# Performance work log

Hardware: AMD Instinct MI355X
Metric: run time of the kernel (lower is better)

Reference implementation:

```python
import jax, jax.numpy as jnp
import numpy as np

B, T, F, H = 256, 128, 512, 512

def setup_inputs() -> dict:
    key = jax.random.key(0)
    ks = jax.random.split(key, 6)
    s_in = 1.0 / np.sqrt(F)
    s_rec = 1.0 / np.sqrt(H)
    return {
        "x": jax.random.normal(ks[0], (B, T, F), dtype=jnp.float32),
        "kernel": jax.random.uniform(ks[1], (F, 3 * H), jnp.float32, -s_in, s_in),
        "rec_kernel": jax.random.uniform(ks[2], (H, 3 * H), jnp.float32, -s_rec, s_rec),
        "bias": jnp.zeros((2, 3 * H), dtype=jnp.float32),  # [input_bias, recurrent_bias] (reset_after=True)
        "Wd": jax.random.uniform(ks[3], (H, 1), jnp.float32, -s_rec, s_rec),
        "bd": jnp.zeros((1,), dtype=jnp.float32),
    }

def reference(x, kernel, rec_kernel, bias, Wd, bd):
    # Keras GRU, reset_after=True, activation=relu, recurrent_activation=sigmoid.
    bi, br = bias[0], bias[1]
    # Precompute all input projections: [T, B, 3H]
    xp = jnp.swapaxes(jnp.einsum('btf,fg->btg', x, kernel) + bi, 0, 1)
    h0 = jnp.zeros((x.shape[0], rec_kernel.shape[0]), dtype=x.dtype)

    def step(h, xp_t):
        rec = h @ rec_kernel + br                  # [B, 3H]
        xz, xr, xh = jnp.split(xp_t, 3, axis=-1)
        rz, rr, rh = jnp.split(rec, 3, axis=-1)
        z = jax.nn.sigmoid(xz + rz)                # update gate
        r = jax.nn.sigmoid(xr + rr)                # reset gate
        hh = jax.nn.relu(xh + r * rh)              # candidate (relu activation)
        h_new = z * h + (1.0 - z) * hh
        return h_new, None

    hT, _ = jax.lax.scan(step, h0, xp)
    # Dropout(0.2) is identity at inference. Dense head:
    return hT @ Wd + bd
```

## Files before the change

kernel.cpp:

```cpp
#include <hip/hip_runtime.h>
#include <hip/hip_bf16.h>
#include <math.h>

constexpr int BATCH = 256;
constexpr int SEQ   = 128;
constexpr int FEAT  = 512;
constexpr int HID   = 512;
constexpr int G3    = 1536;

typedef __bf16 bf16x8 __attribute__((ext_vector_type(8)));
typedef float  f32x4  __attribute__((ext_vector_type(4)));
typedef int    i32x4v __attribute__((ext_vector_type(4)));

__global__ __launch_bounds__(256) void convert_bf16(
    const float* __restrict__ in, __hip_bfloat16* __restrict__ out, int n)
{
  int i = (blockIdx.x * 256 + threadIdx.x) * 8;
  if (i >= n) return;
  float4 v0 = *(const float4*)&in[i];
  float4 v1 = *(const float4*)&in[i + 4];
  __hip_bfloat16 o[8];
  o[0] = (__hip_bfloat16)v0.x; o[1] = (__hip_bfloat16)v0.y;
  o[2] = (__hip_bfloat16)v0.z; o[3] = (__hip_bfloat16)v0.w;
  o[4] = (__hip_bfloat16)v1.x; o[5] = (__hip_bfloat16)v1.y;
  o[6] = (__hip_bfloat16)v1.z; o[7] = (__hip_bfloat16)v1.w;
  *(int4*)&out[i] = *(int4*)o;
}

__global__ __launch_bounds__(256) void transpose_convert(
    const float* __restrict__ in, __hip_bfloat16* __restrict__ outT)
{
  __shared__ float tile[32][33];
  const int c0 = blockIdx.x * 32;
  const int r0 = blockIdx.y * 32;
  const int tid = threadIdx.x;
  {
    int row = tid >> 3, c4 = tid & 7;
    float4 v = *(const float4*)&in[(size_t)(r0 + row) * G3 + c0 + c4 * 4];
    tile[row][c4 * 4 + 0] = v.x;
    tile[row][c4 * 4 + 1] = v.y;
    tile[row][c4 * 4 + 2] = v.z;
    tile[row][c4 * 4 + 3] = v.w;
  }
  __syncthreads();
  {
    int rowT = tid >> 3, c4 = tid & 7;
    __hip_bfloat16 o[4];
#pragma unroll
    for (int e = 0; e < 4; ++e)
      o[e] = (__hip_bfloat16)tile[c4 * 4 + e][rowT];
    *(int2*)&outT[(size_t)(c0 + rowT) * FEAT + r0 + c4 * 4] = *(int2*)o;
  }
}

__global__ __launch_bounds__(256, 3) void proj_mfma(
    const __hip_bfloat16* __restrict__ xb, const __hip_bfloat16* __restrict__ WkT,
    const float* __restrict__ bias, __hip_bfloat16* __restrict__ xp)
{
  __shared__ __align__(16) __hip_bfloat16 As[128 * 64];
  __shared__ __align__(16) __hip_bfloat16 Bs[128 * 64];

  const int tid = threadIdx.x;
  const int wave = tid >> 6, l = tid & 63;
  const int wm = wave >> 1, wn = wave & 1;
  const int m0 = blockIdx.y * 128;
  const int n0 = blockIdx.x * 128;
  const int lr = l & 15, lh = l >> 4;
  const int swz = lr & 7;

  const int srow = l >> 3;
  const int schk = l & 7;
  const int wrow = wave * 32;

  f32x4 acc[4][4] = {};

  for (int k0 = 0; k0 < FEAT; k0 += 64) {
    __syncthreads();
#pragma unroll
    for (int i = 0; i < 4; ++i) {
      int r = wrow + i * 8 + srow;
      const __hip_bfloat16* srcA = &xb[(size_t)(m0 + r) * FEAT + k0 + ((schk ^ srow) * 8)];
      __builtin_amdgcn_global_load_lds(
          (const __attribute__((address_space(1))) void*)srcA,
          (__attribute__((address_space(3))) void*)&As[(wrow + i * 8) * 64], 16, 0, 0);
    }
#pragma unroll
    for (int i = 0; i < 4; ++i) {
      int r = wrow + i * 8 + srow;
      const __hip_bfloat16* srcB = &WkT[(size_t)(n0 + r) * FEAT + k0 + ((schk ^ srow) * 8)];
      __builtin_amdgcn_global_load_lds(
          (const __attribute__((address_space(1))) void*)srcB,
          (__attribute__((address_space(3))) void*)&Bs[(wrow + i * 8) * 64], 16, 0, 0);
    }
    __syncthreads();

#pragma unroll
    for (int ks = 0; ks < 2; ++ks) {
      bf16x8 a[4], b[4];
#pragma unroll
      for (int i = 0; i < 4; ++i) {
        int row = wm * 64 + i * 16 + lr;
        a[i] = *(const bf16x8*)&As[row * 64 + (((ks * 4 + lh) ^ swz) * 8)];
      }
#pragma unroll
      for (int j = 0; j < 4; ++j) {
        int row = wn * 64 + j * 16 + lr;
        b[j] = *(const bf16x8*)&Bs[row * 64 + (((ks * 4 + lh) ^ swz) * 8)];
      }
#pragma unroll
      for (int i = 0; i < 4; ++i)
#pragma unroll
        for (int j = 0; j < 4; ++j)
          acc[i][j] = __builtin_amdgcn_mfma_f32_16x16x32_bf16(a[i], b[j], acc[i][j], 0, 0, 0);
    }
  }

  float bv[4];
#pragma unroll
  for (int j = 0; j < 4; ++j)
    bv[j] = bias[n0 + wn * 64 + j * 16 + lr];
#pragma unroll
  for (int i = 0; i < 4; ++i)
#pragma unroll
    for (int j = 0; j < 4; ++j) {
      int n = n0 + wn * 64 + j * 16 + lr;
#pragma unroll
      for (int r = 0; r < 4; ++r) {
        int m = m0 + wm * 64 + i * 16 + lh * 4 + r;
        xp[(size_t)m * G3 + n] = (__hip_bfloat16)(acc[i][j][r] + bv[j]);
      }
    }
}

__global__ __launch_bounds__(256, 1) void gru_persist(
    __hip_bfloat16* __restrict__ hbA, __hip_bfloat16* __restrict__ hbB,
    float* __restrict__ h32,
    const __hip_bfloat16* __restrict__ xp,
    const __hip_bfloat16* __restrict__ WrT,
    const float* __restrict__ br,
    int* slots)
{
  __shared__ float red[2 * 16 * 100];

  const int tid = threadIdx.x;
  const int bt = blockIdx.x & 15;
  const int jt = blockIdx.x >> 4;
  const int wave = tid >> 6, l = tid & 63;
  const int kh = wave & 1, ch = wave >> 1;
  const int lr = l & 15, lh = l >> 4;

  bf16x8 wfrag[8][3];
#pragma unroll
  for (int f = 0; f < 3; ++f) {
    int r = ch * 48 + f * 16 + lr;
    int n = (r >> 5) * HID + jt * 32 + (r & 31);
    const __hip_bfloat16* wp = &WrT[(size_t)n * HID + kh * 256 + lh * 8];
#pragma unroll
    for (int ks = 0; ks < 8; ++ks)
      wfrag[ks][f] = *(const bf16x8*)&wp[ks * 32];
  }
  asm volatile(""
      : "+v"(wfrag[0][0]), "+v"(wfrag[0][1]), "+v"(wfrag[0][2]),
        "+v"(wfrag[1][0]), "+v"(wfrag[1][1]), "+v"(wfrag[1][2]),
        "+v"(wfrag[2][0]), "+v"(wfrag[2][1]), "+v"(wfrag[2][2]),
        "+v"(wfrag[3][0]), "+v"(wfrag[3][1]), "+v"(wfrag[3][2]),
        "+v"(wfrag[4][0]), "+v"(wfrag[4][1]), "+v"(wfrag[4][2]),
        "+v"(wfrag[5][0]), "+v"(wfrag[5][1]), "+v"(wfrag[5][2]),
        "+v"(wfrag[6][0]), "+v"(wfrag[6][1]), "+v"(wfrag[6][2]),
        "+v"(wfrag[7][0]), "+v"(wfrag[7][1]), "+v"(wfrag[7][2]));

  const int m = tid >> 4, q4 = tid & 15;
  const int b = bt * 16 + m;
  const int jl0 = q4 * 2;
  const int jg0 = jt * 32 + jl0;
  float brz[2], brr[2], brh[2], hreg[2];
#pragma unroll
  for (int p = 0; p < 2; ++p) {
    brz[p] = br[jg0 + p];
    brr[p] = br[HID + jg0 + p];
    brh[p] = br[2 * HID + jg0 + p];
    hreg[p] = 0.f;
  }

  unsigned int uz, ur_, uh_;
  {
    const __hip_bfloat16* xq = &xp[((size_t)b * SEQ + 0) * G3 + jg0];
    uz  = *(const unsigned int*)&xq[0];
    ur_ = *(const unsigned int*)&xq[HID];
    uh_ = *(const unsigned int*)&xq[2 * HID];
  }

  const char* baseA = (const char*)hbA + ((size_t)(bt * 16 + lr) * HID + kh * 256 + lh * 8) * 2;
  const char* baseB = (const char*)hbB + ((size_t)(bt * 16 + lr) * HID + kh * 256 + lh * 8) * 2;

  for (int t = 0; t < SEQ; ++t) {
    const char* hp = (t & 1) ? baseB : baseA;
    __hip_bfloat16* nxt = (t & 1) ? hbA : hbB;

    i32x4v r0, r1, r2, r3, r4, r5, r6, r7;
    asm volatile(
        "global_load_dwordx4 %0, %8, off sc0 sc1\n\t"
        "global_load_dwordx4 %1, %8, off offset:64 sc0 sc1\n\t"
        "global_load_dwordx4 %2, %8, off offset:128 sc0 sc1\n\t"
        "global_load_dwordx4 %3, %8, off offset:192 sc0 sc1\n\t"
        "global_load_dwordx4 %4, %8, off offset:256 sc0 sc1\n\t"
        "global_load_dwordx4 %5, %8, off offset:320 sc0 sc1\n\t"
        "global_load_dwordx4 %6, %8, off offset:384 sc0 sc1\n\t"
        "global_load_dwordx4 %7, %8, off offset:448 sc0 sc1\n\t"
        "s_waitcnt vmcnt(0)"
        : "=&v"(r0), "=&v"(r1), "=&v"(r2), "=&v"(r3),
          "=&v"(r4), "=&v"(r5), "=&v"(r6), "=&v"(r7)
        : "v"(hp)
        : "memory");
    union { i32x4v q; bf16x8 v; } u0, u1, u2, u3, u4, u5, u6, u7;
    u0.q = r0; u1.q = r1; u2.q = r2; u3.q = r3;
    u4.q = r4; u5.q = r5; u6.q = r6; u7.q = r7;
    bf16x8 afrag[8] = {u0.v, u1.v, u2.v, u3.v, u4.v, u5.v, u6.v, u7.v};

    f32x4 acc[3] = {};
#pragma unroll
    for (int ks = 0; ks < 8; ++ks)
#pragma unroll
      for (int f = 0; f < 3; ++f)
        acc[f] = __builtin_amdgcn_mfma_f32_16x16x32_bf16(afrag[ks], wfrag[ks][f], acc[f], 0, 0, 0);

#pragma unroll
    for (int f = 0; f < 3; ++f)
#pragma unroll
      for (int i = 0; i < 4; ++i)
        red[kh * 1600 + (lh * 4 + i) * 100 + ch * 48 + f * 16 + lr] = acc[f][i];
    __syncthreads();

    {
      float xzv[2], xrv[2], xhv[2];
      xzv[0] = (float)((__hip_bfloat16*)&uz)[0];  xzv[1] = (float)((__hip_bfloat16*)&uz)[1];
      xrv[0] = (float)((__hip_bfloat16*)&ur_)[0]; xrv[1] = (float)((__hip_bfloat16*)&ur_)[1];
      xhv[0] = (float)((__hip_bfloat16*)&uh_)[0]; xhv[1] = (float)((__hip_bfloat16*)&uh_)[1];
      float hn[2];
#pragma unroll
      for (int p = 0; p < 2; ++p) {
        int jl = jl0 + p;
        float rz = red[m * 100 + jl]      + red[1600 + m * 100 + jl];
        float rr = red[m * 100 + 32 + jl] + red[1600 + m * 100 + 32 + jl];
        float rh = red[m * 100 + 64 + jl] + red[1600 + m * 100 + 64 + jl];
        rz += brz[p]; rr += brr[p]; rh += brh[p];
        float z  = 1.f / (1.f + __expf(-(xzv[p] + rz)));
        float rg = 1.f / (1.f + __expf(-(xrv[p] + rr)));
        float hh = fmaxf(xhv[p] + rg * rh, 0.f);
        hn[p] = z * hreg[p] + (1.f - z) * hh;
        hreg[p] = hn[p];
      }
      if (t < SEQ - 1) {
        __hip_bfloat16 h0 = (__hip_bfloat16)hn[0], h1 = (__hip_bfloat16)hn[1];
        unsigned int pk = (unsigned int)*(unsigned short*)&h0 |
                          ((unsigned int)*(unsigned short*)&h1 << 16);
        __hip_atomic_store(
            (unsigned int*)&nxt[(size_t)b * HID + jg0], pk,
            __ATOMIC_RELAXED, __HIP_MEMORY_SCOPE_AGENT);
      }
    }

    if (t < SEQ - 1) {
      __syncthreads();

      {
        const __hip_bfloat16* xq = &xp[((size_t)b * SEQ + t + 1) * G3 + jg0];
        uz  = *(const unsigned int*)&xq[0];
        ur_ = *(const unsigned int*)&xq[HID];
        uh_ = *(const unsigned int*)&xq[2 * HID];
      }

      if (tid == 0) {
        __hip_atomic_store(&slots[bt * 16 + jt], t + 1,
                           __ATOMIC_RELAXED, __HIP_MEMORY_SCOPE_AGENT);
        const char* fl = (const char*)&slots[bt * 16];
        for (;;) {
          i32x4v p0, p1, p2, p3;
          asm volatile(
              "global_load_dwordx4 %0, %4, off sc0 sc1\n\t"
              "global_load_dwordx4 %1, %4, off offset:16 sc0 sc1\n\t"
              "global_load_dwordx4 %2, %4, off offset:32 sc0 sc1\n\t"
              "global_load_dwordx4 %3, %4, off offset:48 sc0 sc1\n\t"
              "s_waitcnt vmcnt(0)"
              : "=&v"(p0), "=&v"(p1), "=&v"(p2), "=&v"(p3)
              : "v"(fl)
              : "memory");
          int t1 = t + 1;
          int ok = (p0[0] >= t1) & (p0[1] >= t1) & (p0[2] >= t1) & (p0[3] >= t1) &
                   (p1[0] >= t1) & (p1[1] >= t1) & (p1[2] >= t1) & (p1[3] >= t1) &
                   (p2[0] >= t1) & (p2[1] >= t1) & (p2[2] >= t1) & (p2[3] >= t1) &
                   (p3[0] >= t1) & (p3[1] >= t1) & (p3[2] >= t1) & (p3[3] >= t1);
          if (ok) break;
          __builtin_amdgcn_s_sleep(1);
        }
      }
      __syncthreads();
    }
  }

#pragma unroll
  for (int p = 0; p < 2; ++p)
    h32[(size_t)b * HID + jg0 + p] = hreg[p];
}

__global__ __launch_bounds__(64) void head_kernel(
    const float* __restrict__ h32, const float* __restrict__ Wd,
    const float* __restrict__ bd, float* __restrict__ out)
{
  int b = blockIdx.x, l = threadIdx.x;
  const float* hr = &h32[(size_t)b * HID];
  float s = 0.f;
#pragma unroll
  for (int i = 0; i < 8; ++i)
    s += hr[l + i * 64] * Wd[l + i * 64];
#pragma unroll
  for (int off = 32; off; off >>= 1) s += __shfl_down(s, off);
  if (l == 0) out[b] = s + bd[0];
}

extern "C" void kernel_launch(void* const* d_in, const int* in_sizes, int n_in,
                              void* d_out, int out_size, void* d_ws, size_t ws_size,
                              hipStream_t stream) {
  const float* x    = (const float*)d_in[0];
  const float* Wk   = (const float*)d_in[1];
  const float* Wr   = (const float*)d_in[2];
  const float* bias = (const float*)d_in[3];
  const float* Wd   = (const float*)d_in[4];
  const float* bd   = (const float*)d_in[5];
  float* out = (float*)d_out;

  char* ws = (char*)d_ws;
  size_t off = 0;
  __hip_bfloat16* xp  = (__hip_bfloat16*)(ws + off); off += (size_t)BATCH * SEQ * G3 * 2;
  __hip_bfloat16* xb  = (__hip_bfloat16*)(ws + off); off += (size_t)BATCH * SEQ * FEAT * 2;
  __hip_bfloat16* WkT = (__hip_bfloat16*)(ws + off); off += (size_t)G3 * FEAT * 2;
  __hip_bfloat16* WrT = (__hip_bfloat16*)(ws + off); off += (size_t)G3 * HID * 2;
  float*          h32 = (float*)(ws + off);          off += (size_t)BATCH * HID * 4;
  __hip_bfloat16* hb0 = (__hip_bfloat16*)(ws + off); off += (size_t)BATCH * HID * 2;
  __hip_bfloat16* hb1 = (__hip_bfloat16*)(ws + off); off += (size_t)BATCH * HID * 2;
  int*            slots = (int*)(ws + off);          off += 16 * 16 * sizeof(int);

  convert_bf16<<<(BATCH * SEQ * FEAT) / (256 * 8), 256, 0, stream>>>(x, xb, BATCH * SEQ * FEAT);
  transpose_convert<<<dim3(G3 / 32, FEAT / 32), 256, 0, stream>>>(Wk, WkT);
  transpose_convert<<<dim3(G3 / 32, HID  / 32), 256, 0, stream>>>(Wr, WrT);

  proj_mfma<<<dim3(G3 / 128, (BATCH * SEQ) / 128), 256, 0, stream>>>(xb, WkT, bias, xp);

  hipMemsetAsync(hb0, 0, (size_t)BATCH * HID * sizeof(__hip_bfloat16), stream);
  hipMemsetAsync(slots, 0, 16 * 16 * sizeof(int), stream);

  const float* br = bias + G3;
  {
    void* args[] = {(void*)&hb0, (void*)&hb1, (void*)&h32, (void*)&xp,
                    (void*)&WrT, (void*)&br, (void*)&slots};
    hipLaunchCooperativeKernel((void*)gru_persist, dim3(256), dim3(256),
                               args, 0, stream);
  }

  head_kernel<<<256, 64, 0, stream>>>(h32, Wd, bd, out);
}
```

Before: 458.9 us.

## Split persistent GRU across 512 blocks with 16 hidden columns each and 4-way K split

```diff
diff --git a/kernel.cpp b/kernel.cpp
--- a/kernel.cpp
+++ b/kernel.cpp
@@ -132,7 +132,7 @@
     }
 }
 
-__global__ __launch_bounds__(256, 1) void gru_persist(
+__global__ __launch_bounds__(256, 2) void gru_persist(
     __hip_bfloat16* __restrict__ hbA, __hip_bfloat16* __restrict__ hbB,
     float* __restrict__ h32,
     const __hip_bfloat16* __restrict__ xp,
@@ -140,86 +140,67 @@
     const float* __restrict__ br,
     int* slots)
 {
-  __shared__ float red[2 * 16 * 100];
+  __shared__ float red[4][16][49];
 
   const int tid = threadIdx.x;
   const int bt = blockIdx.x & 15;
   const int jt = blockIdx.x >> 4;
   const int wave = tid >> 6, l = tid & 63;
-  const int kh = wave & 1, ch = wave >> 1;
   const int lr = l & 15, lh = l >> 4;
 
-  bf16x8 wfrag[8][3];
+  bf16x8 wfrag[4][3];
 #pragma unroll
   for (int f = 0; f < 3; ++f) {
-    int r = ch * 48 + f * 16 + lr;
-    int n = (r >> 5) * HID + jt * 32 + (r & 31);
-    const __hip_bfloat16* wp = &WrT[(size_t)n * HID + kh * 256 + lh * 8];
-#pragma unroll
-    for (int ks = 0; ks < 8; ++ks)
+    int n = f * HID + jt * 16 + lr;
+    const __hip_bfloat16* wp = &WrT[(size_t)n * HID + wave * 128 + lh * 8];
+#pragma unroll
+    for (int ks = 0; ks < 4; ++ks)
       wfrag[ks][f] = *(const bf16x8*)&wp[ks * 32];
   }
   asm volatile(""
       : "+v"(wfrag[0][0]), "+v"(wfrag[0][1]), "+v"(wfrag[0][2]),
         "+v"(wfrag[1][0]), "+v"(wfrag[1][1]), "+v"(wfrag[1][2]),
         "+v"(wfrag[2][0]), "+v"(wfrag[2][1]), "+v"(wfrag[2][2]),
-        "+v"(wfrag[3][0]), "+v"(wfrag[3][1]), "+v"(wfrag[3][2]),
-        "+v"(wfrag[4][0]), "+v"(wfrag[4][1]), "+v"(wfrag[4][2]),
-        "+v"(wfrag[5][0]), "+v"(wfrag[5][1]), "+v"(wfrag[5][2]),
-        "+v"(wfrag[6][0]), "+v"(wfrag[6][1]), "+v"(wfrag[6][2]),
-        "+v"(wfrag[7][0]), "+v"(wfrag[7][1]), "+v"(wfrag[7][2]));
-
-  const int m = tid >> 4, q4 = tid & 15;
+        "+v"(wfrag[3][0]), "+v"(wfrag[3][1]), "+v"(wfrag[3][2]));
+
+  const int m = tid >> 4, c = tid & 15;
   const int b = bt * 16 + m;
-  const int jl0 = q4 * 2;
-  const int jg0 = jt * 32 + jl0;
-  float brz[2], brr[2], brh[2], hreg[2];
-#pragma unroll
-  for (int p = 0; p < 2; ++p) {
-    brz[p] = br[jg0 + p];
-    brr[p] = br[HID + jg0 + p];
-    brh[p] = br[2 * HID + jg0 + p];
-    hreg[p] = 0.f;
-  }
-
-  unsigned int uz, ur_, uh_;
+  const int jg = jt * 16 + c;
+  const float brz = br[jg], brr = br[HID + jg], brh = br[2 * HID + jg];
+  float hreg = 0.f;
+
+  float xz, xr, xh;
   {
-    const __hip_bfloat16* xq = &xp[((size_t)b * SEQ + 0) * G3 + jg0];
-    uz  = *(const unsigned int*)&xq[0];
-    ur_ = *(const unsigned int*)&xq[HID];
-    uh_ = *(const unsigned int*)&xq[2 * HID];
-  }
-
-  const char* baseA = (const char*)hbA + ((size_t)(bt * 16 + lr) * HID + kh * 256 + lh * 8) * 2;
-  const char* baseB = (const char*)hbB + ((size_t)(bt * 16 + lr) * HID + kh * 256 + lh * 8) * 2;
+    const __hip_bfloat16* xq = &xp[((size_t)b * SEQ + 0) * G3 + jg];
+    xz = (float)xq[0];
+    xr = (float)xq[HID];
+    xh = (float)xq[2 * HID];
+  }
+
+  const char* baseA = (const char*)hbA + ((size_t)(bt * 16 + lr) * HID + wave * 128 + lh * 8) * 2;
+  const char* baseB = (const char*)hbB + ((size_t)(bt * 16 + lr) * HID + wave * 128 + lh * 8) * 2;
 
   for (int t = 0; t < SEQ; ++t) {
     const char* hp = (t & 1) ? baseB : baseA;
     __hip_bfloat16* nxt = (t & 1) ? hbA : hbB;
 
-    i32x4v r0, r1, r2, r3, r4, r5, r6, r7;
+    i32x4v r0, r1, r2, r3;
     asm volatile(
-        "global_load_dwordx4 %0, %8, off sc0 sc1\n\t"
-        "global_load_dwordx4 %1, %8, off offset:64 sc0 sc1\n\t"
-        "global_load_dwordx4 %2, %8, off offset:128 sc0 sc1\n\t"
-        "global_load_dwordx4 %3, %8, off offset:192 sc0 sc1\n\t"
-        "global_load_dwordx4 %4, %8, off offset:256 sc0 sc1\n\t"
-        "global_load_dwordx4 %5, %8, off offset:320 sc0 sc1\n\t"
-        "global_load_dwordx4 %6, %8, off offset:384 sc0 sc1\n\t"
-        "global_load_dwordx4 %7, %8, off offset:448 sc0 sc1\n\t"
+        "global_load_dwordx4 %0, %4, off sc0 sc1\n\t"
+        "global_load_dwordx4 %1, %4, off offset:64 sc0 sc1\n\t"
+        "global_load_dwordx4 %2, %4, off offset:128 sc0 sc1\n\t"
+        "global_load_dwordx4 %3, %4, off offset:192 sc0 sc1\n\t"
         "s_waitcnt vmcnt(0)"
-        : "=&v"(r0), "=&v"(r1), "=&v"(r2), "=&v"(r3),
-          "=&v"(r4), "=&v"(r5), "=&v"(r6), "=&v"(r7)
+        : "=&v"(r0), "=&v"(r1), "=&v"(r2), "=&v"(r3)
         : "v"(hp)
         : "memory");
-    union { i32x4v q; bf16x8 v; } u0, u1, u2, u3, u4, u5, u6, u7;
+    union { i32x4v q; bf16x8 v; } u0, u1, u2, u3;
     u0.q = r0; u1.q = r1; u2.q = r2; u3.q = r3;
-    u4.q = r4; u5.q = r5; u6.q = r6; u7.q = r7;
-    bf16x8 afrag[8] = {u0.v, u1.v, u2.v, u3.v, u4.v, u5.v, u6.v, u7.v};
+    bf16x8 afrag[4] = {u0.v, u1.v, u2.v, u3.v};
 
     f32x4 acc[3] = {};
 #pragma unroll
-    for (int ks = 0; ks < 8; ++ks)
+    for (int ks = 0; ks < 4; ++ks)
 #pragma unroll
       for (int f = 0; f < 3; ++f)
         acc[f] = __builtin_amdgcn_mfma_f32_16x16x32_bf16(afrag[ks], wfrag[ks][f], acc[f], 0, 0, 0);
@@ -228,68 +209,64 @@
     for (int f = 0; f < 3; ++f)
 #pragma unroll
       for (int i = 0; i < 4; ++i)
-        red[kh * 1600 + (lh * 4 + i) * 100 + ch * 48 + f * 16 + lr] = acc[f][i];
+        red[wave][lh * 4 + i][f * 16 + lr] = acc[f][i];
     __syncthreads();
 
     {
-      float xzv[2], xrv[2], xhv[2];
-      xzv[0] = (float)((__hip_bfloat16*)&uz)[0];  xzv[1] = (float)((__hip_bfloat16*)&uz)[1];
-      xrv[0] = (float)((__hip_bfloat16*)&ur_)[0]; xrv[1] = (float)((__hip_bfloat16*)&ur_)[1];
-      xhv[0] = (float)((__hip_bfloat16*)&uh_)[0]; xhv[1] = (float)((__hip_bfloat16*)&uh_)[1];
-      float hn[2];
-#pragma unroll
-      for (int p = 0; p < 2; ++p) {
-        int jl = jl0 + p;
-        float rz = red[m * 100 + jl]      + red[1600 + m * 100 + jl];
-        float rr = red[m * 100 + 32 + jl] + red[1600 + m * 100 + 32 + jl];
-        float rh = red[m * 100 + 64 + jl] + red[1600 + m * 100 + 64 + jl];
-        rz += brz[p]; rr += brr[p]; rh += brh[p];
-        float z  = 1.f / (1.f + __expf(-(xzv[p] + rz)));
-        float rg = 1.f / (1.f + __expf(-(xrv[p] + rr)));
-        float hh = fmaxf(xhv[p] + rg * rh, 0.f);
-        hn[p] = z * hreg[p] + (1.f - z) * hh;
-        hreg[p] = hn[p];
-      }
+      float rz = red[0][m][c]      + red[1][m][c]      + red[2][m][c]      + red[3][m][c];
+      float rr = red[0][m][16 + c] + red[1][m][16 + c] + red[2][m][16 + c] + red[3][m][16 + c];
+      float rh = red[0][m][32 + c] + red[1][m][32 + c] + red[2][m][32 + c] + red[3][m][32 + c];
+      rz += brz; rr += brr; rh += brh;
+      float z  = 1.f / (1.f + __expf(-(xz + rz)));
+      float rg = 1.f / (1.f + __expf(-(xr + rr)));
+      float hh = fmaxf(xh + rg * rh, 0.f);
+      hreg = z * hreg + (1.f - z) * hh;
+
       if (t < SEQ - 1) {
-        __hip_bfloat16 h0 = (__hip_bfloat16)hn[0], h1 = (__hip_bfloat16)hn[1];
-        unsigned int pk = (unsigned int)*(unsigned short*)&h0 |
-                          ((unsigned int)*(unsigned short*)&h1 << 16);
+        __hip_bfloat16 h0 = (__hip_bfloat16)hreg;
         __hip_atomic_store(
-            (unsigned int*)&nxt[(size_t)b * HID + jg0], pk,
+            (unsigned short*)&nxt[(size_t)b * HID + jg],
+            *(unsigned short*)&h0,
             __ATOMIC_RELAXED, __HIP_MEMORY_SCOPE_AGENT);
+
+        const __hip_bfloat16* xq = &xp[((size_t)b * SEQ + t + 1) * G3 + jg];
+        xz = (float)xq[0];
+        xr = (float)xq[HID];
+        xh = (float)xq[2 * HID];
       }
     }
 
     if (t < SEQ - 1) {
       __syncthreads();
-
-      {
-        const __hip_bfloat16* xq = &xp[((size_t)b * SEQ + t + 1) * G3 + jg0];
-        uz  = *(const unsigned int*)&xq[0];
-        ur_ = *(const unsigned int*)&xq[HID];
-        uh_ = *(const unsigned int*)&xq[2 * HID];
-      }
-
       if (tid == 0) {
-        __hip_atomic_store(&slots[bt * 16 + jt], t + 1,
+        __hip_atomic_store(&slots[bt * 32 + jt], t + 1,
                            __ATOMIC_RELAXED, __HIP_MEMORY_SCOPE_AGENT);
-        const char* fl = (const char*)&slots[bt * 16];
+        const char* fl = (const char*)&slots[bt * 32];
         for (;;) {
-          i32x4v p0, p1, p2, p3;
+          i32x4v p0, p1, p2, p3, p4, p5, p6, p7;
           asm volatile(
-              "global_load_dwordx4 %0, %4, off sc0 sc1\n\t"
-              "global_load_dwordx4 %1, %4, off offset:16 sc0 sc1\n\t"
-              "global_load_dwordx4 %2, %4, off offset:32 sc0 sc1\n\t"
-              "global_load_dwordx4 %3, %4, off offset:48 sc0 sc1\n\t"
+              "global_load_dwordx4 %0, %8, off sc0 sc1\n\t"
+              "global_load_dwordx4 %1, %8, off offset:16 sc0 sc1\n\t"
+              "global_load_dwordx4 %2, %8, off offset:32 sc0 sc1\n\t"
+              "global_load_dwordx4 %3, %8, off offset:48 sc0 sc1\n\t"
+              "global_load_dwordx4 %4, %8, off offset:64 sc0 sc1\n\t"
+              "global_load_dwordx4 %5, %8, off offset:80 sc0 sc1\n\t"
+              "global_load_dwordx4 %6, %8, off offset:96 sc0 sc1\n\t"
+              "global_load_dwordx4 %7, %8, off offset:112 sc0 sc1\n\t"
               "s_waitcnt vmcnt(0)"
-              : "=&v"(p0), "=&v"(p1), "=&v"(p2), "=&v"(p3)
+              : "=&v"(p0), "=&v"(p1), "=&v"(p2), "=&v"(p3),
+                "=&v"(p4), "=&v"(p5), "=&v"(p6), "=&v"(p7)
               : "v"(fl)
               : "memory");
           int t1 = t + 1;
           int ok = (p0[0] >= t1) & (p0[1] >= t1) & (p0[2] >= t1) & (p0[3] >= t1) &
                    (p1[0] >= t1) & (p1[1] >= t1) & (p1[2] >= t1) & (p1[3] >= t1) &
                    (p2[0] >= t1) & (p2[1] >= t1) & (p2[2] >= t1) & (p2[3] >= t1) &
-                   (p3[0] >= t1) & (p3[1] >= t1) & (p3[2] >= t1) & (p3[3] >= t1);
+                   (p3[0] >= t1) & (p3[1] >= t1) & (p3[2] >= t1) & (p3[3] >= t1) &
+                   (p4[0] >= t1) & (p4[1] >= t1) & (p4[2] >= t1) & (p4[3] >= t1) &
+                   (p5[0] >= t1) & (p5[1] >= t1) & (p5[2] >= t1) & (p5[3] >= t1) &
+                   (p6[0] >= t1) & (p6[1] >= t1) & (p6[2] >= t1) & (p6[3] >= t1) &
+                   (p7[0] >= t1) & (p7[1] >= t1) & (p7[2] >= t1) & (p7[3] >= t1);
           if (ok) break;
           __builtin_amdgcn_s_sleep(1);
         }
@@ -298,9 +275,7 @@
     }
   }
 
-#pragma unroll
-  for (int p = 0; p < 2; ++p)
-    h32[(size_t)b * HID + jg0 + p] = hreg[p];
+  h32[(size_t)b * HID + jg] = hreg;
 }
 
 __global__ __launch_bounds__(64) void head_kernel(
@@ -338,7 +313,7 @@
   float*          h32 = (float*)(ws + off);          off += (size_t)BATCH * HID * 4;
   __hip_bfloat16* hb0 = (__hip_bfloat16*)(ws + off); off += (size_t)BATCH * HID * 2;
   __hip_bfloat16* hb1 = (__hip_bfloat16*)(ws + off); off += (size_t)BATCH * HID * 2;
-  int*            slots = (int*)(ws + off);          off += 16 * 16 * sizeof(int);
+  int*            slots = (int*)(ws + off);          off += 16 * 32 * sizeof(int);
 
   convert_bf16<<<(BATCH * SEQ * FEAT) / (256 * 8), 256, 0, stream>>>(x, xb, BATCH * SEQ * FEAT);
   transpose_convert<<<dim3(G3 / 32, FEAT / 32), 256, 0, stream>>>(Wk, WkT);
@@ -347,13 +322,13 @@
   proj_mfma<<<dim3(G3 / 128, (BATCH * SEQ) / 128), 256, 0, stream>>>(xb, WkT, bias, xp);
 
   hipMemsetAsync(hb0, 0, (size_t)BATCH * HID * sizeof(__hip_bfloat16), stream);
-  hipMemsetAsync(slots, 0, 16 * 16 * sizeof(int), stream);
+  hipMemsetAsync(slots, 0, 16 * 32 * sizeof(int), stream);
 
   const float* br = bias + G3;
   {
     void* args[] = {(void*)&hb0, (void*)&hb1, (void*)&h32, (void*)&xp,
                     (void*)&WrT, (void*)&br, (void*)&slots};
-    hipLaunchCooperativeKernel((void*)gru_persist, dim3(256), dim3(256),
+    hipLaunchCooperativeKernel((void*)gru_persist, dim3(512), dim3(256),
                                args, 0, stream);
   }
 
```

Measured after the change: 753.2 us. 1.64x slower.
